# Kernel tuning notes

Measured on AMD Instinct MI355X. Metric: run time of the kernel, lower is better.

Reference implementation:

```python
import jax, jax.numpy as jnp
import numpy as np

B = 4096
D_INPUT = 20
CTX = 10
IN_DIM = CTX * (D_INPUT + 1) + D_INPUT  # 230
D_MODEL = 256
N_LAYERS = 12
D_STATE = 16
D_CONV = 4
EXPAND = 2
D_INNER = EXPAND * D_MODEL  # 512
DT_RANK = (D_MODEL + 15) // 16  # ceil(256/16) = 16


def setup_inputs() -> dict:
    key = jax.random.key(0)
    ks = jax.random.split(key, 12)
    s = lambda k, shape, scale=0.02: jax.random.normal(k, shape, jnp.float32) * scale
    A = jnp.broadcast_to(jnp.arange(1, D_STATE + 1, dtype=jnp.float32), (N_LAYERS, D_INNER, D_STATE))
    return {
        "x": jax.random.normal(ks[0], (B, IN_DIM), jnp.float32),
        "Wi": s(ks[1], (IN_DIM, D_MODEL)),
        "bi": jnp.zeros((D_MODEL,), jnp.float32),
        "in_proj_w": s(ks[2], (N_LAYERS, D_MODEL, 2 * D_INNER)),
        "conv_w": s(ks[3], (N_LAYERS, D_INNER, D_CONV), 0.3),
        "conv_b": jnp.zeros((N_LAYERS, D_INNER), jnp.float32),
        "x_proj_w": s(ks[4], (N_LAYERS, D_INNER, DT_RANK + 2 * D_STATE)),
        "dt_proj_w": s(ks[5], (N_LAYERS, DT_RANK, D_INNER), 0.1),
        "dt_proj_b": jnp.full((N_LAYERS, D_INNER), -4.6, jnp.float32),  # softplus -> small dt
        "A_log": jnp.log(A),  # S4D-real init as in mamba_ssm
        "D": jnp.ones((N_LAYERS, D_INNER), jnp.float32),
        "out_proj_w": s(ks[6], (N_LAYERS, D_INNER, D_MODEL)),
        "Wo": s(ks[7], (D_MODEL, 1)),
        "bo": jnp.zeros((1,), jnp.float32),
    }


def _mamba_block(h, in_proj, conv_w, conv_b, x_proj, dt_w, dt_b, A_log, Dp, out_proj):
    # h: (B, L, D_MODEL)
    Bn, L, _ = h.shape
    xz = h @ in_proj                       # (B, L, 2*D_INNER)
    xr, z = jnp.split(xz, 2, axis=-1)
    # causal depthwise conv1d, kernel D_CONV, left-pad D_CONV-1
    xp = jnp.pad(xr, ((0, 0), (D_CONV - 1, 0), (0, 0)))
    win = jnp.stack([xp[:, k:k + L, :] for k in range(D_CONV)], axis=-1)  # (B,L,C,K)
    xc = jnp.einsum('blck,ck->blc', win, conv_w) + conv_b
    xc = jax.nn.silu(xc)
    dbl = xc @ x_proj                      # (B, L, DT_RANK + 2*D_STATE)
    dt, Bm, Cm = jnp.split(dbl, [DT_RANK, DT_RANK + D_STATE], axis=-1)
    dt = jax.nn.softplus(dt @ dt_w + dt_b)  # (B, L, D_INNER)
    A = -jnp.exp(A_log)                     # (D_INNER, D_STATE)
    dA = jnp.exp(dt[..., None] * A)                              # (B,L,di,ds)
    dBu = dt[..., None] * Bm[:, :, None, :] * xc[..., None]      # (B,L,di,ds)

    def step(hs, inp):
        dA_t, dBu_t, C_t = inp
        hs = dA_t * hs + dBu_t             # (B, di, ds)
        y_t = jnp.einsum('bds,bs->bd', hs, C_t)
        return hs, y_t

    h0 = jnp.zeros((Bn, D_INNER, D_STATE), h.dtype)
    _, ys = jax.lax.scan(step, h0, (dA.swapaxes(0, 1), dBu.swapaxes(0, 1), Cm.swapaxes(0, 1)))
    y = ys.swapaxes(0, 1)                  # (B, L, D_INNER)
    y = y + xc * Dp
    y = y * jax.nn.silu(z)
    return y @ out_proj                    # (B, L, D_MODEL)


def reference(x, Wi, bi, in_proj_w, conv_w, conv_b, x_proj_w, dt_proj_w, dt_proj_b, A_log, D, out_proj_w, Wo, bo):
    h = (x @ Wi + bi)[:, None, :]          # (B, 1, D_MODEL) -- unsqueeze(1)
    for i in range(N_LAYERS):
        h = _mamba_block(h, in_proj_w[i], conv_w[i], conv_b[i], x_proj_w[i],
                         dt_proj_w[i], dt_proj_b[i], A_log[i], D[i], out_proj_w[i])
    h = h[:, 0, :]                         # squeeze(1)
    return h @ Wo + bo                     # (B, 1)
```

## Files before the change

kernel.cpp:

```cpp
#include <hip/hip_runtime.h>
#include <hip/hip_fp8.h>
#include <math.h>

#define NB 4096
#define IN_D 230
#define DM 256
#define NL 12
#define DST 16
#define DI 512
#define DTR 16
#define XPN 48
#define XB 528
#define HB 272

typedef __attribute__((ext_vector_type(4))) float floatx4;
typedef __attribute__((ext_vector_type(2))) float floatx2;
typedef __attribute__((ext_vector_type(2))) long long2v;
typedef __attribute__((ext_vector_type(4))) int intx4;
typedef __attribute__((ext_vector_type(8))) int intx8;

__device__ __forceinline__ float silu_f(float x) {
    return x * __builtin_amdgcn_rcpf(1.0f + __expf(-x));
}
__device__ __forceinline__ float softplus_f(float x) {
    return (x > 20.0f) ? x : __logf(1.0f + __expf(x));
}

__device__ __forceinline__ unsigned char f2fp8(float x) {
#if __has_builtin(__builtin_amdgcn_cvt_pk_fp8_f32)
    return (unsigned char)(__builtin_amdgcn_cvt_pk_fp8_f32(x, x, 0, false) & 0xff);
#else
    __hip_fp8_e4m3 t(x); return (unsigned char)t.__x;
#endif
}
__device__ __forceinline__ unsigned pk4fp8(float a, float b, float c, float d) {
    unsigned w = __builtin_amdgcn_cvt_pk_fp8_f32(a, b, 0, false);
    return __builtin_amdgcn_cvt_pk_fp8_f32(c, d, w, true);
}
template<int S>
__device__ __forceinline__ float fp8sel(unsigned w) {
    return __builtin_amdgcn_cvt_f32_fp8((int)w, S);
}
__device__ __forceinline__ void up4fp8(unsigned w, float* o) {
#if __has_builtin(__builtin_amdgcn_cvt_pk_f32_fp8)
    floatx2 lo = __builtin_amdgcn_cvt_pk_f32_fp8((int)w, false);
    floatx2 hi = __builtin_amdgcn_cvt_pk_f32_fp8((int)w, true);
    o[0] = lo.x; o[1] = lo.y; o[2] = hi.x; o[3] = hi.y;
#else
    o[0] = fp8sel<0>(w); o[1] = fp8sel<1>(w); o[2] = fp8sel<2>(w); o[3] = fp8sel<3>(w);
#endif
}

__device__ __forceinline__ unsigned f2fp4(float x) {
    float ax = fabsf(x);
    unsigned s = (x < 0.0f) ? 8u : 0u;
    unsigned m;
    if      (ax < 0.25f) m = 0;
    else if (ax < 0.75f) m = 1;
    else if (ax < 1.25f) m = 2;
    else if (ax < 1.75f) m = 3;
    else if (ax < 2.50f) m = 4;
    else if (ax < 3.50f) m = 5;
    else if (ax < 5.00f) m = 6;
    else                 m = 7;
    return s | m;
}

__global__ __launch_bounds__(256) void pack_all(
    const float* __restrict__ x,
    const float* __restrict__ Wi, const float* __restrict__ ip,
    const float* __restrict__ op, const float* __restrict__ xp,
    const float* __restrict__ dtw,
    const float* __restrict__ cw, const float* __restrict__ cb,
    const float* __restrict__ db, const float* __restrict__ Dv,
    unsigned char* __restrict__ xpad,
    unsigned char* __restrict__ WiT, unsigned char* __restrict__ dtwP,
    unsigned char* __restrict__ ip4, unsigned char* __restrict__ op4,
    unsigned char* __restrict__ xp4,
    floatx2* __restrict__ cwcb, floatx2* __restrict__ dbdv)
{
    __shared__ float tbuf[64][68];
    const int fid = blockIdx.x;

    if (fid < 1264) {
        const float* src; unsigned char* dst;
        int K, N, ngK, t;
        bool isfp4;
        if (fid < 16) {
            src = Wi; dst = WiT; K = IN_D; N = DM; ngK = 4; t = fid; isfp4 = false;
        } else if (fid < 784) {
            int local = fid - 16; int l = local >> 6; t = local & 63;
            K = DM; N = 2 * DI; ngK = 4; isfp4 = true;
            src = ip + (size_t)l * K * N; dst = ip4 + (size_t)l * 131072;
        } else if (fid < 1168) {
            int local = fid - 784; int l = local >> 5; t = local & 31;
            K = DI; N = DM; ngK = 8; isfp4 = true;
            src = op + (size_t)l * K * N; dst = op4 + (size_t)l * 65536;
        } else {
            int local = fid - 1168; int l = local >> 3; t = local & 7;
            K = DI; N = XPN; ngK = 8; isfp4 = true;
            src = xp + (size_t)l * K * N; dst = xp4 + (size_t)l * 16384;
        }
        const int g = t % ngK, nb = t / ngK;
        const int k0 = g * 64, n0 = nb * 64;
        {
            const int t4 = threadIdx.x;
#pragma unroll
            for (int i = 0; i < 4; i++) {
                int fi = i * 256 + t4;
                int lr = fi >> 4;
                int lc = (fi & 15) * 4;
                int kk = k0 + lr, nn = n0 + lc;
                floatx4 v;
                if (kk < K && nn + 3 < N) {
                    v = *(const floatx4*)(src + (size_t)kk * N + nn);
                } else {
#pragma unroll
                    for (int j = 0; j < 4; j++)
                        v[j] = (kk < K && nn + j < N) ? src[(size_t)kk * N + nn + j] : 0.0f;
                }
                *(floatx4*)(&tbuf[lr][lc]) = v;
            }
        }
        __syncthreads();
        if (!isfp4) {
            const int cbi = threadIdx.x >> 6;
            const int lane = threadIdx.x & 63;
            const int q = lane >> 4, m16 = lane & 15;
            const int chunk = (nb * 4 + cbi) * ngK + g;
            union { unsigned char b[16]; intx4 v; } buf;
#pragma unroll
            for (int sub = 0; sub < 2; sub++)
#pragma unroll
                for (int byt = 0; byt < 8; byt++) {
                    int k = sub * 32 + q * 8 + byt;
                    int n = cbi * 16 + m16;
                    buf.b[sub * 8 + byt] = f2fp8(tbuf[k][n]);
                }
            *(intx4*)(dst + (size_t)chunk * 1024 + lane * 16) = buf.v;
        } else {
            const int kg = g >> 1, half = g & 1;
            const int nkg128 = ngK >> 1;
            const int cbi = threadIdx.x >> 6;
            const int rem = threadIdx.x & 63;
            const int q4loc = rem >> 5;
            const int hb = (rem >> 4) & 1;
            const int m16 = rem & 15;
            const int q4 = half * 2 + q4loc;
            const int chunk = (nb * 4 + cbi) * nkg128 + kg;
            const int kb = q4loc * 32 + hb * 16;
            const int nn = cbi * 16 + m16;
            union { unsigned u[2]; long v; } buf;
#if __has_builtin(__builtin_amdgcn_cvt_scalef32_pk_fp4_f32)
            unsigned d0 = 0, d1 = 0;
            d0 = __builtin_amdgcn_cvt_scalef32_pk_fp4_f32(d0, tbuf[kb + 0][nn] * 128.0f, tbuf[kb + 1][nn] * 128.0f, 1.0f, 0);
            d0 = __builtin_amdgcn_cvt_scalef32_pk_fp4_f32(d0, tbuf[kb + 2][nn] * 128.0f, tbuf[kb + 3][nn] * 128.0f, 1.0f, 1);
            d0 = __builtin_amdgcn_cvt_scalef32_pk_fp4_f32(d0, tbuf[kb + 4][nn] * 128.0f, tbuf[kb + 5][nn] * 128.0f, 1.0f, 2);
            d0 = __builtin_amdgcn_cvt_scalef32_pk_fp4_f32(d0, tbuf[kb + 6][nn] * 128.0f, tbuf[kb + 7][nn] * 128.0f, 1.0f, 3);
            d1 = __builtin_amdgcn_cvt_scalef32_pk_fp4_f32(d1, tbuf[kb + 8][nn] * 128.0f, tbuf[kb + 9][nn] * 128.0f, 1.0f, 0);
            d1 = __builtin_amdgcn_cvt_scalef32_pk_fp4_f32(d1, tbuf[kb + 10][nn] * 128.0f, tbuf[kb + 11][nn] * 128.0f, 1.0f, 1);
            d1 = __builtin_amdgcn_cvt_scalef32_pk_fp4_f32(d1, tbuf[kb + 12][nn] * 128.0f, tbuf[kb + 13][nn] * 128.0f, 1.0f, 2);
            d1 = __builtin_amdgcn_cvt_scalef32_pk_fp4_f32(d1, tbuf[kb + 14][nn] * 128.0f, tbuf[kb + 15][nn] * 128.0f, 1.0f, 3);
            buf.u[0] = d0; buf.u[1] = d1;
#else
            union { unsigned char b[8]; long v; } bb;
#pragma unroll
            for (int bl = 0; bl < 8; bl++) {
                unsigned ob = 0;
#pragma unroll
                for (int i = 0; i < 2; i++) {
                    float v = tbuf[kb + bl * 2 + i][nn] * 128.0f;
                    ob |= f2fp4(v) << (i * 4);
                }
                bb.b[bl] = (unsigned char)ob;
            }
            buf.v = bb.v;
#endif
            *(long*)(dst + (size_t)chunk * 1024 + (q4 * 16 + m16) * 16 + hb * 8) = buf.v;
        }
    } else if (fid < 1456) {
        int gid = (fid - 1264) * 256 + threadIdx.x;
        int idx = gid * 4;
        int l = idx >> 14;
        int r14 = idx & 16383;
        int chunk = r14 >> 9;
        int rr = r14 & 511;
        int lane = rr >> 3, byt0 = rr & 7;
        int q = lane >> 4, m16 = lane & 15;
        int col = chunk * 16 + m16;
        float v[4];
#pragma unroll
        for (int j = 0; j < 4; j++) {
            int k = q * 8 + byt0 + j;
            v[j] = (k < DTR) ? dtw[(size_t)l * DTR * DI + (size_t)k * DI + col] : 0.0f;
        }
        *(unsigned*)(dtwP + idx) = pk4fp8(v[0], v[1], v[2], v[3]);
    } else if (fid < 1480) {
        int idx = (fid - 1456) * 256 + threadIdx.x;
        floatx2 v; v.x = cw[(size_t)idx * 4 + 3]; v.y = cb[idx];
        cwcb[idx] = v;
    } else if (fid < 1504) {
        int idx = (fid - 1480) * 256 + threadIdx.x;
        floatx2 v; v.x = db[idx]; v.y = Dv[idx];
        dbdv[idx] = v;
    } else {
        int gid = (fid - 1504) * 256 + threadIdx.x;
        int r = gid >> 6, c4 = (gid & 63) * 4;
        float v[4];
#pragma unroll
        for (int j = 0; j < 4; j++) {
            int k = c4 + j;
            v[j] = (k < IN_D) ? x[(size_t)r * IN_D + k] : 0.0f;
        }
        *(unsigned*)(xpad + (size_t)gid * 4) = pk4fp8(v[0], v[1], v[2], v[3]);
    }
}

__global__ __launch_bounds__(1024) void mamba_all(
    const unsigned char* __restrict__ xpad, const unsigned char* __restrict__ WiT,
    const float* __restrict__ bi,
    const unsigned char* __restrict__ ip4, const unsigned char* __restrict__ op4,
    const unsigned char* __restrict__ xp4, const unsigned char* __restrict__ dtwP,
    const floatx2* __restrict__ cwcb, const floatx2* __restrict__ dbdv,
    const float* __restrict__ Wo, const float* __restrict__ bo,
    float* __restrict__ out)
{
    __shared__ unsigned char hs[16 * HB];
    __shared__ unsigned char xcs[16 * XB];
    __shared__ unsigned char szs[16 * XB];
    __shared__ float dbls[16 * 68];

    const int tid = threadIdx.x;
    const int w = tid >> 6, lane = tid & 63;
    const int q = lane >> 4, m16 = lane & 15;
    const int rb = blockIdx.x * 16;
    const long2v z2 = (long2v){0, 0};

    {
        floatx4 a0 = (floatx4){0.f, 0.f, 0.f, 0.f};
        floatx4 a1 = (floatx4){0.f, 0.f, 0.f, 0.f};
        const unsigned char* Bp = xpad + (size_t)(rb + m16) * DM + q * 8;
        const unsigned char* Ap = WiT + (size_t)(w * 4) * 1024 + lane * 16;
#pragma unroll
        for (int g = 0; g < 4; g++) {
            long2v a = *(const long2v*)(Ap + g * 1024);
            long bv0 = *(const long*)(Bp + (g * 2) * 32);
            long bv1 = *(const long*)(Bp + (g * 2 + 1) * 32);
            a0 = __builtin_amdgcn_mfma_f32_16x16x32_fp8_fp8(a.x, bv0, a0, 0, 0, 0);
            a1 = __builtin_amdgcn_mfma_f32_16x16x32_fp8_fp8(a.y, bv1, a1, 0, 0, 0);
        }
        a0 = a0 + a1;
        floatx4 b4 = *(const floatx4*)(bi + w * 16 + q * 4);
        *(unsigned*)(hs + m16 * HB + w * 16 + q * 4) =
            pk4fp8(a0[0] + b4[0], a0[1] + b4[1], a0[2] + b4[2], a0[3] + b4[3]);
    }
    __syncthreads();

    for (int l = 0; l < NL; l++) {
        const unsigned char* ipw = ip4 + (size_t)l * 131072;
        const unsigned char* xpw = xp4 + (size_t)l * 16384;
        const unsigned char* opw = op4 + (size_t)l * 65536;
        const unsigned char* dwp = dtwP + (size_t)l * 16384;
        const floatx2* cc = cwcb + (size_t)l * DI;
        const floatx2* dd = dbdv + (size_t)l * DI;

        long2v a2[4];
        if (w < 4) {
            const unsigned char* Ap2 = xpw + (size_t)(w * 4) * 1024 + lane * 16;
#pragma unroll
            for (int i = 0; i < 4; i++) a2[i] = *(const long2v*)(Ap2 + (size_t)i * 1024);
        }
        long w3a, w3b;
        {
            const unsigned char* Wp = dwp + (size_t)(w * 2) * 512 + lane * 8;
            w3a = *(const long*)(Wp);
            w3b = *(const long*)(Wp + 512);
        }
        long2v a4[4];
        {
            const unsigned char* Ap4 = opw + (size_t)(w * 4) * 1024 + lane * 16;
#pragma unroll
            for (int i = 0; i < 4; i++) a4[i] = *(const long2v*)(Ap4 + (size_t)i * 1024);
        }

        {
            floatx4 acc[4];
#pragma unroll
            for (int t = 0; t < 4; t++) acc[t] = (floatx4){0.f, 0.f, 0.f, 0.f};
            const unsigned char* Ap = ipw + (size_t)(w * 8) * 1024 + lane * 16;
            const unsigned char* Br = hs + m16 * HB + q * 32;
#pragma unroll
            for (int kg = 0; kg < 2; kg++) {
                union { long2v h[2]; intx8 v; } bv;
                bv.h[0] = *(const long2v*)(Br + kg * 128);
                bv.h[1] = *(const long2v*)(Br + kg * 128 + 16);
#pragma unroll
                for (int t = 0; t < 4; t++) {
                    union { long2v h[2]; intx8 v; } av;
                    av.h[0] = *(const long2v*)(Ap + (size_t)(t * 2 + kg) * 1024);
                    av.h[1] = z2;
                    acc[t] = __builtin_amdgcn_mfma_scale_f32_16x16x128_f8f6f4(
                        av.v, bv.v, acc[t], 4, 0, 0, 120, 0, 127);
                }
            }
            if (w < 8) {
#pragma unroll
                for (int t = 0; t < 4; t++) {
                    int colb = w * 64 + t * 16 + q * 4;
                    floatx4 cA = *(const floatx4*)(cc + colb);
                    floatx4 cB = *(const floatx4*)(cc + colb + 2);
                    float v0 = silu_f(acc[t][0] * cA[0] + cA[1]);
                    float v1 = silu_f(acc[t][1] * cA[2] + cA[3]);
                    float v2 = silu_f(acc[t][2] * cB[0] + cB[1]);
                    float v3 = silu_f(acc[t][3] * cB[2] + cB[3]);
                    *(unsigned*)(xcs + m16 * XB + colb) = pk4fp8(v0, v1, v2, v3);
                }
            } else {
#pragma unroll
                for (int t = 0; t < 4; t++) {
                    int colb = (w - 8) * 64 + t * 16 + q * 4;
                    *(unsigned*)(szs + m16 * XB + colb) =
                        pk4fp8(silu_f(acc[t][0]), silu_f(acc[t][1]),
                               silu_f(acc[t][2]), silu_f(acc[t][3]));
                }
            }
        }
        __syncthreads();

        if (w < 4) {
            floatx4 acc = (floatx4){0.f, 0.f, 0.f, 0.f};
            const unsigned char* Br = xcs + m16 * XB + q * 32;
#pragma unroll
            for (int kg = 0; kg < 4; kg++) {
                union { long2v h[2]; intx8 v; } bv;
                bv.h[0] = *(const long2v*)(Br + kg * 128);
                bv.h[1] = *(const long2v*)(Br + kg * 128 + 16);
                union { long2v h[2]; intx8 v; } av;
                av.h[0] = a2[kg];
                av.h[1] = z2;
                acc = __builtin_amdgcn_mfma_scale_f32_16x16x128_f8f6f4(
                    av.v, bv.v, acc, 4, 0, 0, 120, 0, 127);
            }
            *(floatx4*)(&dbls[m16 * 68 + w * 16 + q * 4]) = acc;
        }
        __syncthreads();

        {
            const int cb0 = w * 32 + q * 4;

            const int brow = lane >> 2, bj = lane & 3;
            const float* dr0 = &dbls[brow * 68 + DTR];
            float p = dr0[bj]      * dr0[DST + bj]
                    + dr0[bj + 4]  * dr0[DST + bj + 4]
                    + dr0[bj + 8]  * dr0[DST + bj + 8]
                    + dr0[bj + 12] * dr0[DST + bj + 12];
            p += __shfl_xor(p, 1);
            p += __shfl_xor(p, 2);
            float bcv = __shfl(p, m16 * 4);

            long bfrag = 0;
            if (q < 2) {
                const float* dr = &dbls[m16 * 68 + q * 8];
                union { unsigned u[2]; long l; } uv;
                uv.u[0] = pk4fp8(dr[0], dr[1], dr[2], dr[3]);
                uv.u[1] = pk4fp8(dr[4], dr[5], dr[6], dr[7]);
                bfrag = uv.l;
            }

            floatx4 dA = *(const floatx4*)(dd + cb0);
            floatx4 dB = *(const floatx4*)(dd + cb0 + 2);
            floatx4 dC = *(const floatx4*)(dd + cb0 + 16);
            floatx4 dD = *(const floatx4*)(dd + cb0 + 18);
            floatx4 d0v = (floatx4){dA[0], dA[2], dB[0], dB[2]};
            floatx4 d1v = (floatx4){dC[0], dC[2], dD[0], dD[2]};
            floatx4 Dv0 = (floatx4){dA[1], dA[3], dB[1], dB[3]};
            floatx4 Dv1 = (floatx4){dC[1], dC[3], dD[1], dD[3]};
            d0v = __builtin_amdgcn_mfma_f32_16x16x32_fp8_fp8(w3a, bfrag, d0v, 0, 0, 0);
            d1v = __builtin_amdgcn_mfma_f32_16x16x32_fp8_fp8(w3b, bfrag, d1v, 0, 0, 0);

            const int off = m16 * XB + cb0;
            unsigned xw0 = *(const unsigned*)(xcs + off);
            unsigned zw0 = *(const unsigned*)(szs + off);
            unsigned xw1 = *(const unsigned*)(xcs + off + 16);
            unsigned zw1 = *(const unsigned*)(szs + off + 16);
            float xf0[4], zf0[4], xf1[4], zf1[4];
            up4fp8(xw0, xf0); up4fp8(zw0, zf0);
            up4fp8(xw1, xf1); up4fp8(zw1, zf1);
            float y0[4], y1[4];
#pragma unroll
            for (int r = 0; r < 4; r++) {
                y0[r] = (softplus_f(d0v[r]) * bcv + Dv0[r]) * xf0[r] * zf0[r];
                y1[r] = (softplus_f(d1v[r]) * bcv + Dv1[r]) * xf1[r] * zf1[r];
            }
            *(unsigned*)(xcs + off)      = pk4fp8(y0[0], y0[1], y0[2], y0[3]);
            *(unsigned*)(xcs + off + 16) = pk4fp8(y1[0], y1[1], y1[2], y1[3]);
        }
        __syncthreads();

        {
            floatx4 acc = (floatx4){0.f, 0.f, 0.f, 0.f};
            const unsigned char* Br = xcs + m16 * XB + q * 32;
#pragma unroll
            for (int kg = 0; kg < 4; kg++) {
                union { long2v h[2]; intx8 v; } bv;
                bv.h[0] = *(const long2v*)(Br + kg * 128);
                bv.h[1] = *(const long2v*)(Br + kg * 128 + 16);
                union { long2v h[2]; intx8 v; } av;
                av.h[0] = a4[kg];
                av.h[1] = z2;
                acc = __builtin_amdgcn_mfma_scale_f32_16x16x128_f8f6f4(
                    av.v, bv.v, acc, 4, 0, 0, 120, 0, 127);
            }
            *(unsigned*)(hs + m16 * HB + w * 16 + q * 4) =
                pk4fp8(acc[0], acc[1], acc[2], acc[3]);
        }
        __syncthreads();
    }

    {
        unsigned hw = *(const unsigned*)(hs + w * HB + lane * 4);
        floatx4 w4 = *(const floatx4*)(Wo + lane * 4);
        float hf[4];
        up4fp8(hw, hf);
        float s = hf[0] * w4[0] + hf[1] * w4[1] + hf[2] * w4[2] + hf[3] * w4[3];
#pragma unroll
        for (int off = 32; off > 0; off >>= 1) s += __shfl_down(s, off);
        if (lane == 0) out[rb + w] = s + bo[0];
    }
}

extern "C" void kernel_launch(void* const* d_in, const int* in_sizes, int n_in,
                              void* d_out, int out_size, void* d_ws, size_t ws_size,
                              hipStream_t stream)
{
    const float* x       = (const float*)d_in[0];
    const float* Wi      = (const float*)d_in[1];
    const float* bi      = (const float*)d_in[2];
    const float* in_proj = (const float*)d_in[3];
    const float* conv_w  = (const float*)d_in[4];
    const float* conv_b  = (const float*)d_in[5];
    const float* x_proj  = (const float*)d_in[6];
    const float* dt_w    = (const float*)d_in[7];
    const float* dt_b    = (const float*)d_in[8];
    const float* Dp      = (const float*)d_in[10];
    const float* out_pw  = (const float*)d_in[11];
    const float* Wo      = (const float*)d_in[12];
    const float* bo      = (const float*)d_in[13];

    unsigned char* ws = (unsigned char*)d_ws;
    unsigned char* xpad = ws;
    unsigned char* WiT  = xpad + (size_t)NB * DM;
    unsigned char* dtwP = WiT + (size_t)DM * DM;
    floatx2* cwcb = (floatx2*)(dtwP + (size_t)NL * 16384);
    floatx2* dbdv = cwcb + (size_t)NL * DI;
    unsigned char* ip4 = (unsigned char*)(dbdv + (size_t)NL * DI);
    unsigned char* op4 = ip4 + (size_t)NL * 131072;
    unsigned char* xp4 = op4 + (size_t)NL * 65536;

    pack_all<<<dim3(2528), dim3(256), 0, stream>>>(
        x, Wi, in_proj, out_pw, x_proj, dt_w, conv_w, conv_b, dt_b, Dp,
        xpad, WiT, dtwP, ip4, op4, xp4, cwcb, dbdv);

    mamba_all<<<dim3(NB / 16), dim3(1024), 0, stream>>>(
        xpad, WiT, bi, ip4, op4, xp4, dtwP,
        cwcb, dbdv, Wo, bo, (float*)d_out);
}
```

Before: 166.3 us.

## Halve rows per block to 8 and use 512-thread blocks

The fused Mamba kernel now processes 8 batch rows per block with 8 waves instead of 16 rows with 16 waves, launching twice as many blocks. Each wave covers twice as many output columns in every GEMM stage, and the 16-row MFMA tiles keep their shape but only 8 rows are stored. The aim is to let two blocks share a CU so one block's barrier stalls can overlap the other's work. The cost is that half of every MFMA tile's rows is wasted and each block still loads the full per-layer weights, so total MFMA work and weight traffic per batch row both double.

```diff
diff --git a/kernel.cpp b/kernel.cpp
--- a/kernel.cpp
+++ b/kernel.cpp
@@ -216,7 +216,7 @@
     }
 }
 
-__global__ __launch_bounds__(1024) void mamba_all(
+__global__ __launch_bounds__(512, 4) void mamba_all(
     const unsigned char* __restrict__ xpad, const unsigned char* __restrict__ WiT,
     const float* __restrict__ bi,
     const unsigned char* __restrict__ ip4, const unsigned char* __restrict__ op4,
@@ -225,34 +225,42 @@
     const float* __restrict__ Wo, const float* __restrict__ bo,
     float* __restrict__ out)
 {
-    __shared__ unsigned char hs[16 * HB];
-    __shared__ unsigned char xcs[16 * XB];
-    __shared__ unsigned char szs[16 * XB];
-    __shared__ float dbls[16 * 68];
+    __shared__ unsigned char hs[8 * HB];
+    __shared__ unsigned char xcs[8 * XB];
+    __shared__ unsigned char szs[8 * XB];
+    __shared__ float dbls[8 * 68];
 
     const int tid = threadIdx.x;
     const int w = tid >> 6, lane = tid & 63;
     const int q = lane >> 4, m16 = lane & 15;
-    const int rb = blockIdx.x * 16;
+    const int m8 = m16 & 7;
+    const bool rowok = (m16 < 8);
+    const int rb = blockIdx.x * 8;
     const long2v z2 = (long2v){0, 0};
 
     {
-        floatx4 a0 = (floatx4){0.f, 0.f, 0.f, 0.f};
-        floatx4 a1 = (floatx4){0.f, 0.f, 0.f, 0.f};
-        const unsigned char* Bp = xpad + (size_t)(rb + m16) * DM + q * 8;
-        const unsigned char* Ap = WiT + (size_t)(w * 4) * 1024 + lane * 16;
-#pragma unroll
-        for (int g = 0; g < 4; g++) {
-            long2v a = *(const long2v*)(Ap + g * 1024);
-            long bv0 = *(const long*)(Bp + (g * 2) * 32);
-            long bv1 = *(const long*)(Bp + (g * 2 + 1) * 32);
-            a0 = __builtin_amdgcn_mfma_f32_16x16x32_fp8_fp8(a.x, bv0, a0, 0, 0, 0);
-            a1 = __builtin_amdgcn_mfma_f32_16x16x32_fp8_fp8(a.y, bv1, a1, 0, 0, 0);
-        }
-        a0 = a0 + a1;
-        floatx4 b4 = *(const floatx4*)(bi + w * 16 + q * 4);
-        *(unsigned*)(hs + m16 * HB + w * 16 + q * 4) =
-            pk4fp8(a0[0] + b4[0], a0[1] + b4[1], a0[2] + b4[2], a0[3] + b4[3]);
+        const unsigned char* Bp = xpad + (size_t)(rb + m8) * DM + q * 8;
+        const unsigned char* Ap = WiT + (size_t)(w * 8) * 1024 + lane * 16;
+#pragma unroll
+        for (int t = 0; t < 2; t++) {
+            floatx4 a0 = (floatx4){0.f, 0.f, 0.f, 0.f};
+            floatx4 a1 = (floatx4){0.f, 0.f, 0.f, 0.f};
+#pragma unroll
+            for (int g = 0; g < 4; g++) {
+                long2v a = *(const long2v*)(Ap + (size_t)(t * 4 + g) * 1024);
+                long bv0 = *(const long*)(Bp + (g * 2) * 32);
+                long bv1 = *(const long*)(Bp + (g * 2 + 1) * 32);
+                a0 = __builtin_amdgcn_mfma_f32_16x16x32_fp8_fp8(a.x, bv0, a0, 0, 0, 0);
+                a1 = __builtin_amdgcn_mfma_f32_16x16x32_fp8_fp8(a.y, bv1, a1, 0, 0, 0);
+            }
+            a0 = a0 + a1;
+            if (rowok) {
+                int colb = (w * 2 + t) * 16 + q * 4;
+                floatx4 b4 = *(const floatx4*)(bi + colb);
+                *(unsigned*)(hs + m16 * HB + colb) =
+                    pk4fp8(a0[0] + b4[0], a0[1] + b4[1], a0[2] + b4[2], a0[3] + b4[3]);
+            }
+        }
     }
     __syncthreads();
 
@@ -270,58 +278,63 @@
 #pragma unroll
             for (int i = 0; i < 4; i++) a2[i] = *(const long2v*)(Ap2 + (size_t)i * 1024);
         }
-        long w3a, w3b;
-        {
-            const unsigned char* Wp = dwp + (size_t)(w * 2) * 512 + lane * 8;
-            w3a = *(const long*)(Wp);
-            w3b = *(const long*)(Wp + 512);
+        long w3[4];
+        {
+            const unsigned char* Wp = dwp + (size_t)(w * 4) * 512 + lane * 8;
+#pragma unroll
+            for (int j = 0; j < 4; j++) w3[j] = *(const long*)(Wp + (size_t)j * 512);
         }
         long2v a4[4];
         {
-            const unsigned char* Ap4 = opw + (size_t)(w * 4) * 1024 + lane * 16;
+            const unsigned char* Ap4 = opw + (size_t)(w * 8) * 1024 + lane * 16;
 #pragma unroll
             for (int i = 0; i < 4; i++) a4[i] = *(const long2v*)(Ap4 + (size_t)i * 1024);
         }
 
         {
-            floatx4 acc[4];
-#pragma unroll
-            for (int t = 0; t < 4; t++) acc[t] = (floatx4){0.f, 0.f, 0.f, 0.f};
-            const unsigned char* Ap = ipw + (size_t)(w * 8) * 1024 + lane * 16;
-            const unsigned char* Br = hs + m16 * HB + q * 32;
-#pragma unroll
-            for (int kg = 0; kg < 2; kg++) {
-                union { long2v h[2]; intx8 v; } bv;
-                bv.h[0] = *(const long2v*)(Br + kg * 128);
-                bv.h[1] = *(const long2v*)(Br + kg * 128 + 16);
-#pragma unroll
-                for (int t = 0; t < 4; t++) {
-                    union { long2v h[2]; intx8 v; } av;
-                    av.h[0] = *(const long2v*)(Ap + (size_t)(t * 2 + kg) * 1024);
-                    av.h[1] = z2;
-                    acc[t] = __builtin_amdgcn_mfma_scale_f32_16x16x128_f8f6f4(
-                        av.v, bv.v, acc[t], 4, 0, 0, 120, 0, 127);
-                }
-            }
-            if (w < 8) {
-#pragma unroll
-                for (int t = 0; t < 4; t++) {
-                    int colb = w * 64 + t * 16 + q * 4;
-                    floatx4 cA = *(const floatx4*)(cc + colb);
-                    floatx4 cB = *(const floatx4*)(cc + colb + 2);
-                    float v0 = silu_f(acc[t][0] * cA[0] + cA[1]);
-                    float v1 = silu_f(acc[t][1] * cA[2] + cA[3]);
-                    float v2 = silu_f(acc[t][2] * cB[0] + cB[1]);
-                    float v3 = silu_f(acc[t][3] * cB[2] + cB[3]);
-                    *(unsigned*)(xcs + m16 * XB + colb) = pk4fp8(v0, v1, v2, v3);
-                }
-            } else {
-#pragma unroll
-                for (int t = 0; t < 4; t++) {
-                    int colb = (w - 8) * 64 + t * 16 + q * 4;
-                    *(unsigned*)(szs + m16 * XB + colb) =
-                        pk4fp8(silu_f(acc[t][0]), silu_f(acc[t][1]),
-                               silu_f(acc[t][2]), silu_f(acc[t][3]));
+            const unsigned char* Ap = ipw + (size_t)(w * 16) * 1024 + lane * 16;
+            const unsigned char* Br = hs + m8 * HB + q * 32;
+#pragma unroll
+            for (int grp = 0; grp < 2; grp++) {
+                floatx4 acc[4];
+#pragma unroll
+                for (int t = 0; t < 4; t++) acc[t] = (floatx4){0.f, 0.f, 0.f, 0.f};
+#pragma unroll
+                for (int kg = 0; kg < 2; kg++) {
+                    union { long2v h[2]; intx8 v; } bv;
+                    bv.h[0] = *(const long2v*)(Br + kg * 128);
+                    bv.h[1] = *(const long2v*)(Br + kg * 128 + 16);
+#pragma unroll
+                    for (int t = 0; t < 4; t++) {
+                        union { long2v h[2]; intx8 v; } av;
+                        av.h[0] = *(const long2v*)(Ap + (size_t)((grp * 4 + t) * 2 + kg) * 1024);
+                        av.h[1] = z2;
+                        acc[t] = __builtin_amdgcn_mfma_scale_f32_16x16x128_f8f6f4(
+                            av.v, bv.v, acc[t], 4, 0, 0, 120, 0, 127);
+                    }
+                }
+                if (rowok) {
+                    if (w < 4) {
+#pragma unroll
+                        for (int t = 0; t < 4; t++) {
+                            int colb = w * 128 + (grp * 4 + t) * 16 + q * 4;
+                            floatx4 cA = *(const floatx4*)(cc + colb);
+                            floatx4 cB = *(const floatx4*)(cc + colb + 2);
+                            float v0 = silu_f(acc[t][0] * cA[0] + cA[1]);
+                            float v1 = silu_f(acc[t][1] * cA[2] + cA[3]);
+                            float v2 = silu_f(acc[t][2] * cB[0] + cB[1]);
+                            float v3 = silu_f(acc[t][3] * cB[2] + cB[3]);
+                            *(unsigned*)(xcs + m16 * XB + colb) = pk4fp8(v0, v1, v2, v3);
+                        }
+                    } else {
+#pragma unroll
+                        for (int t = 0; t < 4; t++) {
+                            int colb = (w - 4) * 128 + (grp * 4 + t) * 16 + q * 4;
+                            *(unsigned*)(szs + m16 * XB + colb) =
+                                pk4fp8(silu_f(acc[t][0]), silu_f(acc[t][1]),
+                                       silu_f(acc[t][2]), silu_f(acc[t][3]));
+                        }
+                    }
                 }
             }
         }
@@ -329,7 +342,7 @@
 
         if (w < 4) {
             floatx4 acc = (floatx4){0.f, 0.f, 0.f, 0.f};
-            const unsigned char* Br = xcs + m16 * XB + q * 32;
+            const unsigned char* Br = xcs + m8 * XB + q * 32;
 #pragma unroll
             for (int kg = 0; kg < 4; kg++) {
                 union { long2v h[2]; intx8 v; } bv;
@@ -341,14 +354,13 @@
                 acc = __builtin_amdgcn_mfma_scale_f32_16x16x128_f8f6f4(
                     av.v, bv.v, acc, 4, 0, 0, 120, 0, 127);
             }
-            *(floatx4*)(&dbls[m16 * 68 + w * 16 + q * 4]) = acc;
+            if (rowok)
+                *(floatx4*)(&dbls[m16 * 68 + w * 16 + q * 4]) = acc;
         }
         __syncthreads();
 
         {
-            const int cb0 = w * 32 + q * 4;
-
-            const int brow = lane >> 2, bj = lane & 3;
+            const int brow = (lane >> 2) & 7, bj = lane & 3;
             const float* dr0 = &dbls[brow * 68 + DTR];
             float p = dr0[bj]      * dr0[DST + bj]
                     + dr0[bj + 4]  * dr0[DST + bj + 4]
@@ -356,63 +368,74 @@
                     + dr0[bj + 12] * dr0[DST + bj + 12];
             p += __shfl_xor(p, 1);
             p += __shfl_xor(p, 2);
-            float bcv = __shfl(p, m16 * 4);
+            float bcv = __shfl(p, m8 * 4);
 
             long bfrag = 0;
             if (q < 2) {
-                const float* dr = &dbls[m16 * 68 + q * 8];
+                const float* dr = &dbls[m8 * 68 + q * 8];
                 union { unsigned u[2]; long l; } uv;
                 uv.u[0] = pk4fp8(dr[0], dr[1], dr[2], dr[3]);
                 uv.u[1] = pk4fp8(dr[4], dr[5], dr[6], dr[7]);
                 bfrag = uv.l;
             }
 
-            floatx4 dA = *(const floatx4*)(dd + cb0);
-            floatx4 dB = *(const floatx4*)(dd + cb0 + 2);
-            floatx4 dC = *(const floatx4*)(dd + cb0 + 16);
-            floatx4 dD = *(const floatx4*)(dd + cb0 + 18);
-            floatx4 d0v = (floatx4){dA[0], dA[2], dB[0], dB[2]};
-            floatx4 d1v = (floatx4){dC[0], dC[2], dD[0], dD[2]};
-            floatx4 Dv0 = (floatx4){dA[1], dA[3], dB[1], dB[3]};
-            floatx4 Dv1 = (floatx4){dC[1], dC[3], dD[1], dD[3]};
-            d0v = __builtin_amdgcn_mfma_f32_16x16x32_fp8_fp8(w3a, bfrag, d0v, 0, 0, 0);
-            d1v = __builtin_amdgcn_mfma_f32_16x16x32_fp8_fp8(w3b, bfrag, d1v, 0, 0, 0);
-
-            const int off = m16 * XB + cb0;
-            unsigned xw0 = *(const unsigned*)(xcs + off);
-            unsigned zw0 = *(const unsigned*)(szs + off);
-            unsigned xw1 = *(const unsigned*)(xcs + off + 16);
-            unsigned zw1 = *(const unsigned*)(szs + off + 16);
-            float xf0[4], zf0[4], xf1[4], zf1[4];
-            up4fp8(xw0, xf0); up4fp8(zw0, zf0);
-            up4fp8(xw1, xf1); up4fp8(zw1, zf1);
-            float y0[4], y1[4];
-#pragma unroll
-            for (int r = 0; r < 4; r++) {
-                y0[r] = (softplus_f(d0v[r]) * bcv + Dv0[r]) * xf0[r] * zf0[r];
-                y1[r] = (softplus_f(d1v[r]) * bcv + Dv1[r]) * xf1[r] * zf1[r];
-            }
-            *(unsigned*)(xcs + off)      = pk4fp8(y0[0], y0[1], y0[2], y0[3]);
-            *(unsigned*)(xcs + off + 16) = pk4fp8(y1[0], y1[1], y1[2], y1[3]);
+            floatx4 dv[4], Dvv[4];
+#pragma unroll
+            for (int j = 0; j < 4; j++) {
+                const int cbj = w * 64 + j * 16 + q * 4;
+                floatx4 dA = *(const floatx4*)(dd + cbj);
+                floatx4 dB = *(const floatx4*)(dd + cbj + 2);
+                floatx4 db0 = (floatx4){dA[0], dA[2], dB[0], dB[2]};
+                Dvv[j] = (floatx4){dA[1], dA[3], dB[1], dB[3]};
+                dv[j] = __builtin_amdgcn_mfma_f32_16x16x32_fp8_fp8(w3[j], bfrag, db0, 0, 0, 0);
+            }
+            if (rowok) {
+#pragma unroll
+                for (int j = 0; j < 4; j++) {
+                    const int off = m16 * XB + w * 64 + j * 16 + q * 4;
+                    unsigned xw = *(const unsigned*)(xcs + off);
+                    unsigned zw = *(const unsigned*)(szs + off);
+                    float xf[4], zf[4];
+                    up4fp8(xw, xf); up4fp8(zw, zf);
+                    float y[4];
+#pragma unroll
+                    for (int r = 0; r < 4; r++)
+                        y[r] = (softplus_f(dv[j][r]) * bcv + Dvv[j][r]) * xf[r] * zf[r];
+                    *(unsigned*)(xcs + off) = pk4fp8(y[0], y[1], y[2], y[3]);
+                }
+            }
         }
         __syncthreads();
 
         {
-            floatx4 acc = (floatx4){0.f, 0.f, 0.f, 0.f};
-            const unsigned char* Br = xcs + m16 * XB + q * 32;
+            const unsigned char* Ap4b = opw + (size_t)(w * 8 + 4) * 1024 + lane * 16;
+            long2v a4b[4];
+#pragma unroll
+            for (int i = 0; i < 4; i++) a4b[i] = *(const long2v*)(Ap4b + (size_t)i * 1024);
+
+            floatx4 acc0 = (floatx4){0.f, 0.f, 0.f, 0.f};
+            floatx4 acc1 = (floatx4){0.f, 0.f, 0.f, 0.f};
+            const unsigned char* Br = xcs + m8 * XB + q * 32;
 #pragma unroll
             for (int kg = 0; kg < 4; kg++) {
                 union { long2v h[2]; intx8 v; } bv;
                 bv.h[0] = *(const long2v*)(Br + kg * 128);
                 bv.h[1] = *(const long2v*)(Br + kg * 128 + 16);
                 union { long2v h[2]; intx8 v; } av;
+                av.h[1] = z2;
                 av.h[0] = a4[kg];
-                av.h[1] = z2;
-                acc = __builtin_amdgcn_mfma_scale_f32_16x16x128_f8f6f4(
-                    av.v, bv.v, acc, 4, 0, 0, 120, 0, 127);
-            }
-            *(unsigned*)(hs + m16 * HB + w * 16 + q * 4) =
-                pk4fp8(acc[0], acc[1], acc[2], acc[3]);
+                acc0 = __builtin_amdgcn_mfma_scale_f32_16x16x128_f8f6f4(
+                    av.v, bv.v, acc0, 4, 0, 0, 120, 0, 127);
+                av.h[0] = a4b[kg];
+                acc1 = __builtin_amdgcn_mfma_scale_f32_16x16x128_f8f6f4(
+                    av.v, bv.v, acc1, 4, 0, 0, 120, 0, 127);
+            }
+            if (rowok) {
+                *(unsigned*)(hs + m16 * HB + w * 32 + q * 4) =
+                    pk4fp8(acc0[0], acc0[1], acc0[2], acc0[3]);
+                *(unsigned*)(hs + m16 * HB + w * 32 + 16 + q * 4) =
+                    pk4fp8(acc1[0], acc1[1], acc1[2], acc1[3]);
+            }
         }
         __syncthreads();
     }
@@ -461,7 +484,7 @@
         x, Wi, in_proj, out_pw, x_proj, dt_w, conv_w, conv_b, dt_b, Dp,
         xpad, WiT, dtwP, ip4, op4, xp4, cwcb, dbdv);
 
-    mamba_all<<<dim3(NB / 16), dim3(1024), 0, stream>>>(
+    mamba_all<<<dim3(NB / 8), dim3(512), 0, stream>>>(
         xpad, WiT, bi, ip4, op4, xp4, dtwP,
         cwcb, dbdv, Wo, bo, (float*)d_out);
 }
```

Result: slower. 209.7 us (+26.1%).
